# Performance work log

Hardware: AMD Instinct MI355X
Metric: run time of the kernel (lower is better)

The kernel has to match this reference:

```python
import jax, jax.numpy as jnp
import numpy as np

NS, NV = 48, 10            # scalar / vector multiplicities
IN_SIZE = NS + 3*NV + 3*NV + NS   # 156
N_EDGE_FEAT = 96
HIDDEN = 96
# weight shapes per output irrep: 0e:(58,48) 1o:(68,10) 1e:(68,10) 0o:(58,48)
W_SHAPES = [('0e', NS + NV, NS), ('1o', NS + 2*NV, NV), ('1e', 2*NV + NS, NV), ('0o', NV + NS, NS)]
WEIGHT_NUMEL = sum(a*b for _, a, b in W_SHAPES)  # 6928
N_NODES, N_EDGES = 10000, 50000


def setup_inputs() -> dict:
    key = jax.random.key(0)
    ks = jax.random.split(key, 9)
    node_attr = jax.random.normal(ks[0], (N_NODES, IN_SIZE), dtype=jnp.float32)
    edge_index = jax.random.randint(ks[1], (2, N_EDGES), 0, N_NODES)
    edge_attr = jax.random.normal(ks[2], (N_EDGES, N_EDGE_FEAT), dtype=jnp.float32)
    edge_sh = jax.random.normal(ks[3], (N_EDGES, 4), dtype=jnp.float32)
    s1 = 1.0 / np.sqrt(N_EDGE_FEAT)
    s2 = 1.0 / np.sqrt(HIDDEN)
    W1 = jax.random.normal(ks[4], (N_EDGE_FEAT, HIDDEN), dtype=jnp.float32) * s1
    b1 = jnp.zeros((HIDDEN,), dtype=jnp.float32)
    W2 = jax.random.normal(ks[5], (HIDDEN, WEIGHT_NUMEL), dtype=jnp.float32) * s2
    b2 = jnp.zeros((WEIGHT_NUMEL,), dtype=jnp.float32)
    return {'node_attr': node_attr, 'edge_index': edge_index, 'edge_attr': edge_attr,
            'edge_sh': edge_sh, 'W1': W1, 'b1': b1, 'W2': W2, 'b2': b2}


def _faster_tp(in_, sh, weight):
    # in_: [E, 156], sh: [E, 4], weight: [E, 6928]
    in_0e = in_[:, :NS]                                   # [E,48]
    in_1o = in_[:, NS:NS + 3*NV].reshape(-1, NV, 3)       # [E,10,3]
    in_1e = in_[:, NS + 3*NV:NS + 6*NV].reshape(-1, NV, 3)
    in_0o = in_[:, NS + 6*NV:]                            # [E,48]
    sh_0e = sh[:, 0]                                      # [E]
    sh_1o = sh[:, 1:]                                     # [E,3]
    inv_s3 = 1.0 / np.sqrt(3.0)
    inv_s2 = 1.0 / np.sqrt(2.0)

    out_0e = jnp.concatenate([
        in_0e * sh_0e[:, None],
        jnp.sum(in_1o * sh_1o[:, None, :], axis=-1) * inv_s3], axis=-1)      # [E,58]
    out_1o = jnp.concatenate([
        in_0e[:, :, None] * sh_1o[:, None, :],
        in_1o * sh_0e[:, None, None],
        jnp.cross(in_1e, sh_1o[:, None, :]) * inv_s2], axis=-2)              # [E,68,3]
    out_1e = jnp.concatenate([
        jnp.cross(in_1o, sh_1o[:, None, :]) * inv_s2,
        in_1e * sh_0e[:, None, None],
        in_0o[:, :, None] * sh_1o[:, None, :]], axis=-2)                     # [E,68,3]
    out_0o = jnp.concatenate([
        jnp.sum(in_1e * sh_1o[:, None, :], axis=-1) * inv_s3,
        in_0o * sh_0e[:, None]], axis=-1)                                    # [E,58]

    wd = {}
    start = 0
    for name, a, b in W_SHAPES:
        wd[name] = weight[:, start:start + a*b].reshape(-1, a, b) / np.sqrt(a)
        start += a*b

    o0e = jnp.einsum('ei,eio->eo', out_0e, wd['0e'])                 # [E,48]
    o1o = jnp.einsum('eic,eio->eoc', out_1o, wd['1o']).reshape(-1, 3*NV)
    o1e = jnp.einsum('eic,eio->eoc', out_1e, wd['1e']).reshape(-1, 3*NV)
    o0o = jnp.einsum('ei,eio->eo', out_0o, wd['0o'])                 # [E,48]
    return jnp.concatenate([o0e, o1o, o1e, o0o], axis=-1)           # [E,156]


def reference(node_attr, edge_index, edge_attr, edge_sh, W1, b1, W2, b2):
    edge_src, edge_dst = edge_index[0], edge_index[1]
    # edge MLP -> per-edge TP weights
    h = jax.nn.relu(edge_attr @ W1 + b1)
    w = h @ W2 + b2                                       # [E, 6928]
    tp = _faster_tp(node_attr[edge_dst], edge_sh, w)      # [E, 156]
    # scatter-mean over source nodes
    n = node_attr.shape[0]
    seg = jax.ops.segment_sum(tp, edge_src, num_segments=n)
    cnt = jax.ops.segment_sum(jnp.ones((tp.shape[0],), tp.dtype), edge_src, num_segments=n)
    out = seg / jnp.maximum(cnt, 1.0)[:, None]
    # residual (in/out sizes equal, so pad is a no-op)
    return out + node_attr
```

## Files before the change

kernel.cpp:

```cpp
#include <hip/hip_runtime.h>

#define NE 50000
#define NN 10000
#define KH 96
#define WN 6928
#define NTILE 484
#define IN_SZ 156
#define EPW 64

typedef __attribute__((ext_vector_type(8))) short short8;
typedef __attribute__((ext_vector_type(4))) float float4v;

__device__ __forceinline__ unsigned short f2bf(float x) {
  unsigned u = __float_as_uint(x);
  unsigned r = (u + 0x7FFFu + ((u >> 16) & 1u)) >> 16;
  return (unsigned short)r;
}
__device__ __forceinline__ float b2f(unsigned short u) {
  return __uint_as_float(((unsigned)u) << 16);
}

__device__ __forceinline__ void issue3(short8 (&B)[3], float &bv,
                                       const unsigned short* p, const float* pb) {
  asm volatile("global_load_dwordx4 %0, %4, off\n\t"
               "global_load_dwordx4 %1, %4, off offset:1024\n\t"
               "global_load_dwordx4 %2, %4, off offset:2048\n\t"
               "global_load_dword %3, %5, off"
               : "=&v"(B[0]), "=&v"(B[1]), "=&v"(B[2]), "=&v"(bv)
               : "v"(p), "v"(pb));
}
__device__ __forceinline__ void waitB8(short8 (&B)[3], float &bv) {
  asm volatile("s_waitcnt vmcnt(8)"
               : "+v"(B[0]), "+v"(B[1]), "+v"(B[2]), "+v"(bv));
}
__device__ __forceinline__ void waitB4(short8 (&B)[3], float &bv) {
  asm volatile("s_waitcnt vmcnt(4)"
               : "+v"(B[0]), "+v"(B[1]), "+v"(B[2]), "+v"(bv));
}
__device__ __forceinline__ void waitB0(short8 (&B)[3], float &bv) {
  asm volatile("s_waitcnt vmcnt(0)"
               : "+v"(B[0]), "+v"(B[1]), "+v"(B[2]), "+v"(bv));
}

__device__ __forceinline__ int col_of_np(int np) {
  if (np < 2784) return np;
  if (np < 3872) { int rel = np - 2784, i = rel >> 4, o = rel & 15; return (o < 10) ? 2784 + i * 10 + o : -1; }
  if (np < 4960) { int rel = np - 3872, i = rel >> 4, o = rel & 15; return (o < 10) ? 3464 + i * 10 + o : -1; }
  return 4144 + (np - 4960);
}

#define R0 (NTILE * 192)
#define R1 (R0 + NTILE * 16)
#define R2 (R1 + KH * KH)
#define R3 (R2 + NN * IN_SZ / 4)
#define R4 (R3 + NN / 4)
#define R5 (R4 + 576)
__global__ __launch_bounds__(256) void prep_kernel(
    const float* __restrict__ W2, const float* __restrict__ b2,
    const float* __restrict__ W1,
    unsigned short* __restrict__ W2PT, float* __restrict__ b2PT,
    unsigned short* __restrict__ W1T,
    float* __restrict__ acc, int* __restrict__ icnt,
    unsigned short* __restrict__ h_ext)
{
  int gid = blockIdx.x * 256 + threadIdx.x;
  if (gid < R0) {
    int lane = gid & 63, s = (gid >> 6) % 3, t = gid / 192;
    int l = lane & 15, q = lane >> 4;
    int c = col_of_np(t * 16 + l);
    int kbase = s * 32 + q * 8;
    unsigned short o8[8];
    #pragma unroll
    for (int j = 0; j < 8; ++j) {
      int k = kbase + j;
      float v = (c >= 0) ? W2[(size_t)k * WN + c] : 0.f;
      o8[j] = f2bf(v);
    }
    uint4 pk;
    pk.x = o8[0] | ((unsigned)o8[1] << 16);
    pk.y = o8[2] | ((unsigned)o8[3] << 16);
    pk.z = o8[4] | ((unsigned)o8[5] << 16);
    pk.w = o8[6] | ((unsigned)o8[7] << 16);
    *(uint4*)(W2PT + (size_t)gid * 8) = pk;
  } else if (gid < R1) {
    int j = gid - R0;
    int c = col_of_np(j);
    b2PT[j] = (c >= 0) ? b2[c] : 0.f;
  } else if (gid < R2) {
    int j = gid - R1;
    int c = j / KH, k = j - c * KH;
    W1T[c * KH + k] = f2bf(W1[k * KH + c]);
  } else if (gid < R3) {
    uint4 z = {0, 0, 0, 0};
    ((uint4*)acc)[gid - R2] = z;
  } else if (gid < R4) {
    uint4 z = {0, 0, 0, 0};
    ((uint4*)icnt)[gid - R3] = z;
  } else if (gid < R5) {
    uint4 z = {0, 0, 0, 0};
    ((uint4*)(h_ext + (size_t)NE * KH))[gid - R4] = z;
  }
}

__global__ __launch_bounds__(384) void mlp1_kernel(
    const float* __restrict__ edge_attr, const unsigned short* __restrict__ W1T,
    const float* __restrict__ b1, unsigned short* __restrict__ h_ext)
{
  const int tid = threadIdx.x;
  const int e0 = blockIdx.x * 16;
  const int w = tid >> 6, l = tid & 15, q = (tid >> 4) & 3;

  short8 a[3], b[3];
  #pragma unroll
  for (int s = 0; s < 3; ++s) {
    const float* pa = edge_attr + (size_t)(e0 + l) * KH + s * 32 + q * 8;
    float4 x = *(const float4*)pa, y = *(const float4*)(pa + 4);
    short8 t;
    t[0] = (short)f2bf(x.x); t[1] = (short)f2bf(x.y);
    t[2] = (short)f2bf(x.z); t[3] = (short)f2bf(x.w);
    t[4] = (short)f2bf(y.x); t[5] = (short)f2bf(y.y);
    t[6] = (short)f2bf(y.z); t[7] = (short)f2bf(y.w);
    a[s] = t;
    b[s] = *(const short8*)(W1T + (size_t)(w * 16 + l) * KH + s * 32 + q * 8);
  }
  float4v C = {0.f, 0.f, 0.f, 0.f};
  #pragma unroll
  for (int s = 0; s < 3; ++s)
    C = __builtin_amdgcn_mfma_f32_16x16x32_bf16(a[s], b[s], C, 0, 0, 0);

  float bv = b1[w * 16 + l];
  #pragma unroll
  for (int r = 0; r < 4; ++r)
    h_ext[(size_t)(e0 + q * 4 + r) * KH + w * 16 + l] = f2bf(fmaxf(C[r] + bv, 0.f));
}

__global__ __launch_bounds__(512, 2) void tp_kernel(
    const unsigned short* __restrict__ h_ext, const float* __restrict__ node_attr,
    const int* __restrict__ edge_index, const float* __restrict__ edge_sh,
    const unsigned short* __restrict__ W2PT, const float* __restrict__ b2PT,
    float* __restrict__ acc, int* __restrict__ icnt)
{
  __shared__ unsigned short sIn[EPW][160];
  __shared__ float sOut[EPW][IN_SZ];
  __shared__ unsigned short sF0[2][60][EPW];
  __shared__ unsigned short sF1[2][68][3][EPW];
  __shared__ float sShs[EPW][4];
  __shared__ int sSrc[EPW], sDst[EPW];

  const int tid = threadIdx.x;
  const int e0 = blockIdx.x * EPW;

  if (tid < EPW) {
    int ok = (e0 + tid) < NE;
    int s = ok ? edge_index[e0 + tid] : 0;
    int d = ok ? edge_index[NE + e0 + tid] : 0;
    sSrc[tid] = s; sDst[tid] = d;
    if (ok) atomicAdd(&icnt[s], 1);
  }
  if (tid >= 128 && tid < 384) {
    int t2 = tid - 128;
    int e = t2 >> 2, c = t2 & 3;
    sShs[e][c] = ((e0 + e) < NE) ? edge_sh[(size_t)(e0 + e) * 4 + c] : 0.f;
  }
  __syncthreads();

  for (int idx = tid; idx < EPW * IN_SZ; idx += 512) {
    int e = idx / IN_SZ, f = idx - e * IN_SZ;
    sIn[e][f] = f2bf(node_attr[(size_t)sDst[e] * IN_SZ + f]);
  }
  for (int idx = tid; idx < EPW * IN_SZ; idx += 512) (&sOut[0][0])[idx] = 0.f;
  __syncthreads();

  {
    const int e = tid >> 3, j = tid & 7;
    const float sh0 = sShs[e][0], sx = sShs[e][1], sy = sShs[e][2], sz = sShs[e][3];
    const float i3 = 0.57735026918962576f, i2 = 0.70710678118654752f;
    for (int i = j; i < 48; i += 8) {
      float v0 = b2f(sIn[e][i]), w0 = b2f(sIn[e][108 + i]);
      sF0[0][i][e] = f2bf(v0 * sh0);
      sF0[1][10 + i][e] = f2bf(w0 * sh0);
      sF1[0][i][0][e] = f2bf(v0 * sx); sF1[0][i][1][e] = f2bf(v0 * sy); sF1[0][i][2][e] = f2bf(v0 * sz);
      sF1[1][20 + i][0][e] = f2bf(w0 * sx); sF1[1][20 + i][1][e] = f2bf(w0 * sy); sF1[1][20 + i][2][e] = f2bf(w0 * sz);
    }
    for (int v = j; v < 10; v += 8) {
      float ax = b2f(sIn[e][48 + 3 * v]), ay = b2f(sIn[e][48 + 3 * v + 1]), az = b2f(sIn[e][48 + 3 * v + 2]);
      float bx = b2f(sIn[e][78 + 3 * v]), by = b2f(sIn[e][78 + 3 * v + 1]), bz = b2f(sIn[e][78 + 3 * v + 2]);
      sF0[0][48 + v][e] = f2bf((ax * sx + ay * sy + az * sz) * i3);
      sF0[1][v][e]      = f2bf((bx * sx + by * sy + bz * sz) * i3);
      sF1[0][48 + v][0][e] = f2bf(ax * sh0); sF1[0][48 + v][1][e] = f2bf(ay * sh0); sF1[0][48 + v][2][e] = f2bf(az * sh0);
      sF1[0][58 + v][0][e] = f2bf((by * sz - bz * sy) * i2);
      sF1[0][58 + v][1][e] = f2bf((bz * sx - bx * sz) * i2);
      sF1[0][58 + v][2][e] = f2bf((bx * sy - by * sx) * i2);
      sF1[1][v][0][e] = f2bf((ay * sz - az * sy) * i2);
      sF1[1][v][1][e] = f2bf((az * sx - ax * sz) * i2);
      sF1[1][v][2][e] = f2bf((ax * sy - ay * sx) * i2);
      sF1[1][10 + v][0][e] = f2bf(bx * sh0); sF1[1][10 + v][1][e] = f2bf(by * sh0); sF1[1][10 + v][2][e] = f2bf(bz * sh0);
    }
  }
  if (tid < 256) {
    int fam = tid >> 7, i = 58 + ((tid >> 6) & 1), e = tid & 63;
    sF0[fam][i][e] = 0;
  }
  __syncthreads();

  const int wv = tid >> 6, l = tid & 15, q = (tid >> 4) & 3;

  short8 Af[4][3];
  #pragma unroll
  for (int m = 0; m < 4; ++m) {
    const unsigned short* ar = h_ext + (size_t)(e0 + m * 16 + l) * KH + q * 8;
    #pragma unroll
    for (int s = 0; s < 3; ++s) Af[m][s] = *(const short8*)(ar + s * 32);
  }

  const unsigned short* wlane = W2PT + (size_t)(tid & 63) * 8;
  const float* blane = b2PT + l;

  auto sbody = [&](float (&a)[4][4], const short8 (&B)[3], float bv,
                   int sf, int i) {
    ushort4 f0 = *(const ushort4*)&sF0[sf][i][q * 4];
    ushort4 f1 = *(const ushort4*)&sF0[sf][i][16 + q * 4];
    ushort4 f2 = *(const ushort4*)&sF0[sf][i][32 + q * 4];
    ushort4 f3 = *(const ushort4*)&sF0[sf][i][48 + q * 4];
    float4v C0 = {bv, bv, bv, bv}, C1 = C0, C2 = C0, C3 = C0;
    #pragma unroll
    for (int s2 = 0; s2 < 3; ++s2) {
      C0 = __builtin_amdgcn_mfma_f32_16x16x32_bf16(Af[0][s2], B[s2], C0, 0, 0, 0);
      C1 = __builtin_amdgcn_mfma_f32_16x16x32_bf16(Af[1][s2], B[s2], C1, 0, 0, 0);
      C2 = __builtin_amdgcn_mfma_f32_16x16x32_bf16(Af[2][s2], B[s2], C2, 0, 0, 0);
      C3 = __builtin_amdgcn_mfma_f32_16x16x32_bf16(Af[3][s2], B[s2], C3, 0, 0, 0);
    }
    a[0][0] += C0[0] * b2f(f0.x); a[0][1] += C0[1] * b2f(f0.y);
    a[0][2] += C0[2] * b2f(f0.z); a[0][3] += C0[3] * b2f(f0.w);
    a[1][0] += C1[0] * b2f(f1.x); a[1][1] += C1[1] * b2f(f1.y);
    a[1][2] += C1[2] * b2f(f1.z); a[1][3] += C1[3] * b2f(f1.w);
    a[2][0] += C2[0] * b2f(f2.x); a[2][1] += C2[1] * b2f(f2.y);
    a[2][2] += C2[2] * b2f(f2.z); a[2][3] += C2[3] * b2f(f2.w);
    a[3][0] += C3[0] * b2f(f3.x); a[3][1] += C3[1] * b2f(f3.y);
    a[3][2] += C3[2] * b2f(f3.z); a[3][3] += C3[3] * b2f(f3.w);
  };
  auto sflush = [&](float (&a)[4][4], int col) {
    #pragma unroll
    for (int h = 0; h < 4; ++h)
      #pragma unroll
      for (int r = 0; r < 4; ++r)
        unsafeAtomicAdd(&sOut[h * 16 + q * 4 + r][col], a[h][r]);
  };

  if (wv < 4) {
    const int sf = wv >> 1;
    const int ibeg = (wv & 1) * 30;
    const int tb = sf ? 310 : 0;
    const int obase = sf ? 108 : 0;
    #pragma unroll 1
    for (int ob = 0; ob < 3; ++ob) {
      float a[4][4] = {{0.f,0.f,0.f,0.f},{0.f,0.f,0.f,0.f},{0.f,0.f,0.f,0.f},{0.f,0.f,0.f,0.f}};
      short8 Ba[3], Bb[3], Bc[3];
      float vA, vB, vC;
      auto tadr = [&](int ii) -> size_t {
        int i = ibeg + ii; if (i >= 58) i = ibeg;
        return (size_t)(tb + 3 * i + ob);
      };
      { size_t t = tadr(0); issue3(Ba, vA, wlane + t * 1536, blane + t * 16); }
      { size_t t = tadr(1); issue3(Bb, vB, wlane + t * 1536, blane + t * 16); }
      { size_t t = tadr(2); issue3(Bc, vC, wlane + t * 1536, blane + t * 16); }
      #pragma unroll 1
      for (int ii = 0; ii < 27; ii += 3) {
        waitB8(Ba, vA); sbody(a, Ba, vA, sf, ibeg + ii);
        { size_t t = tadr(ii + 3); issue3(Ba, vA, wlane + t * 1536, blane + t * 16); }
        waitB8(Bb, vB); sbody(a, Bb, vB, sf, ibeg + ii + 1);
        { size_t t = tadr(ii + 4); issue3(Bb, vB, wlane + t * 1536, blane + t * 16); }
        waitB8(Bc, vC); sbody(a, Bc, vC, sf, ibeg + ii + 2);
        { size_t t = tadr(ii + 5); issue3(Bc, vC, wlane + t * 1536, blane + t * 16); }
      }
      waitB8(Ba, vA); sbody(a, Ba, vA, sf, ibeg + 27);
      waitB4(Bb, vB); sbody(a, Bb, vB, sf, ibeg + 28);
      waitB0(Bc, vC); sbody(a, Bc, vC, sf, ibeg + 29);
      sflush(a, obase + ob * 16 + l);
    }
  } else {
    const int vf = (wv >> 1) - 2;
    const int ibeg = (wv & 1) * 34;
    const int tb = vf ? 242 : 174;
    float r0[4][3] = {{0.f}}, r1[4][3] = {{0.f}}, r2[4][3] = {{0.f}}, r3[4][3] = {{0.f}};
    short8 Ba[3], Bb[3];
    float vA, vB;
    auto tadr = [&](int ii) -> size_t { return (size_t)(tb + ibeg + ii); };
    auto vbody = [&](const short8 (&B)[3], float bv, int ii) {
      int i = ibeg + ii;
      ushort4 g0[3], g1[3], g2[3], g3[3];
      #pragma unroll
      for (int cc = 0; cc < 3; ++cc) {
        g0[cc] = *(const ushort4*)&sF1[vf][i][cc][q * 4];
        g1[cc] = *(const ushort4*)&sF1[vf][i][cc][16 + q * 4];
        g2[cc] = *(const ushort4*)&sF1[vf][i][cc][32 + q * 4];
        g3[cc] = *(const ushort4*)&sF1[vf][i][cc][48 + q * 4];
      }
      float4v C0 = {bv, bv, bv, bv}, C1 = C0, C2 = C0, C3 = C0;
      #pragma unroll
      for (int s = 0; s < 3; ++s) {
        C0 = __builtin_amdgcn_mfma_f32_16x16x32_bf16(Af[0][s], B[s], C0, 0, 0, 0);
        C1 = __builtin_amdgcn_mfma_f32_16x16x32_bf16(Af[1][s], B[s], C1, 0, 0, 0);
        C2 = __builtin_amdgcn_mfma_f32_16x16x32_bf16(Af[2][s], B[s], C2, 0, 0, 0);
        C3 = __builtin_amdgcn_mfma_f32_16x16x32_bf16(Af[3][s], B[s], C3, 0, 0, 0);
      }
      #pragma unroll
      for (int cc = 0; cc < 3; ++cc) {
        r0[0][cc] += C0[0] * b2f(g0[cc].x); r0[1][cc] += C0[1] * b2f(g0[cc].y);
        r0[2][cc] += C0[2] * b2f(g0[cc].z); r0[3][cc] += C0[3] * b2f(g0[cc].w);
        r1[0][cc] += C1[0] * b2f(g1[cc].x); r1[1][cc] += C1[1] * b2f(g1[cc].y);
        r1[2][cc] += C1[2] * b2f(g1[cc].z); r1[3][cc] += C1[3] * b2f(g1[cc].w);
        r2[0][cc] += C2[0] * b2f(g2[cc].x); r2[1][cc] += C2[1] * b2f(g2[cc].y);
        r2[2][cc] += C2[2] * b2f(g2[cc].z); r2[3][cc] += C2[3] * b2f(g2[cc].w);
        r3[0][cc] += C3[0] * b2f(g3[cc].x); r3[1][cc] += C3[1] * b2f(g3[cc].y);
        r3[2][cc] += C3[2] * b2f(g3[cc].z); r3[3][cc] += C3[3] * b2f(g3[cc].w);
      }
    };
    { size_t t = tadr(0); issue3(Ba, vA, wlane + t * 1536, blane + t * 16); }
    { size_t t = tadr(1); issue3(Bb, vB, wlane + t * 1536, blane + t * 16); }
    #pragma unroll 1
    for (int ii = 0; ii < 32; ii += 2) {
      waitB4(Ba, vA); vbody(Ba, vA, ii);
      { size_t t = tadr(ii + 2); issue3(Ba, vA, wlane + t * 1536, blane + t * 16); }
      waitB4(Bb, vB); vbody(Bb, vB, ii + 1);
      { size_t t = tadr(ii + 3); issue3(Bb, vB, wlane + t * 1536, blane + t * 16); }
    }
    waitB4(Ba, vA); vbody(Ba, vA, 32);
    waitB0(Bb, vB); vbody(Bb, vB, 33);
    if (l < 10) {
      const int col = (vf ? 78 : 48) + 3 * l;
      #pragma unroll
      for (int r = 0; r < 4; ++r)
        #pragma unroll
        for (int cc = 0; cc < 3; ++cc) {
          unsafeAtomicAdd(&sOut[q * 4 + r][col + cc],      r0[r][cc]);
          unsafeAtomicAdd(&sOut[16 + q * 4 + r][col + cc], r1[r][cc]);
          unsafeAtomicAdd(&sOut[32 + q * 4 + r][col + cc], r2[r][cc]);
          unsafeAtomicAdd(&sOut[48 + q * 4 + r][col + cc], r3[r][cc]);
        }
    }
  }
  __syncthreads();

  const float n58 = 0.13130643285972254f, n68 = 0.12126781251816650f;
  for (int idx = tid; idx < EPW * IN_SZ; idx += 512) {
    int e = idx / IN_SZ, o = idx - e * IN_SZ;
    if (e0 + e < NE) {
      float nrm = (o < 48 || o >= 108) ? n58 : n68;
      unsafeAtomicAdd(&acc[(size_t)sSrc[e] * IN_SZ + o], sOut[e][o] * nrm);
    }
  }
}

__global__ __launch_bounds__(256) void finalize_kernel(
    const float* __restrict__ acc, const int* __restrict__ icnt,
    const float* __restrict__ node_attr, float* __restrict__ out)
{
  int idx = blockIdx.x * 256 + threadIdx.x;
  if (idx < NN * IN_SZ) {
    int n = idx / IN_SZ;
    out[idx] = acc[idx] / fmaxf((float)icnt[n], 1.f) + node_attr[idx];
  }
}

extern "C" void kernel_launch(void* const* d_in, const int* in_sizes, int n_in,
                              void* d_out, int out_size, void* d_ws, size_t ws_size,
                              hipStream_t stream)
{
  const float* node_attr  = (const float*)d_in[0];
  const int*   edge_index = (const int*)d_in[1];
  const float* edge_attr  = (const float*)d_in[2];
  const float* edge_sh    = (const float*)d_in[3];
  const float* W1 = (const float*)d_in[4];
  const float* b1 = (const float*)d_in[5];
  const float* W2 = (const float*)d_in[6];
  const float* b2 = (const float*)d_in[7];
  float* out = (float*)d_out;

  unsigned short* h_ext = (unsigned short*)d_ws;
  unsigned short* W2PT  = h_ext + (size_t)50048 * KH;
  float* b2PT = (float*)(W2PT + (size_t)NTILE * 1536);
  float* acc  = b2PT + (size_t)NTILE * 16;
  int*   icnt = (int*)(acc + (size_t)NN * IN_SZ);
  unsigned short* W1T = (unsigned short*)(icnt + NN);

  prep_kernel<<<(R5 + 255) / 256, 256, 0, stream>>>(W2, b2, W1, W2PT, b2PT, W1T,
                                                    acc, icnt, h_ext);
  mlp1_kernel<<<NE / 16, 384, 0, stream>>>(edge_attr, W1T, b1, h_ext);
  tp_kernel<<<(NE + EPW - 1) / EPW, 512, 0, stream>>>(h_ext, node_attr, edge_index,
                                                      edge_sh, W2PT, b2PT, acc, icnt);
  finalize_kernel<<<(NN * IN_SZ + 255) / 256, 256, 0, stream>>>(acc, icnt, node_attr, out);
}
```

Before: 351.3 us.

## Drop shared staging buffers; read node features directly and atomically accumulate to global

Removes the sIn staging of gathered node features and the sOut shared accumulation tile. Features are now read straight from global memory during feature construction, and per-edge partial results are atomically added straight into the global accumulator with normalization applied in registers. Padding edges are routed to an extra dummy row so no bounds check is needed. This cuts shared memory use and a barrier, which may raise occupancy, but it raises global atomic traffic because each output element is now hit from several waves separately.

```diff
diff --git a/kernel.cpp b/kernel.cpp
--- a/kernel.cpp
+++ b/kernel.cpp
@@ -52,7 +52,7 @@
 #define R0 (NTILE * 192)
 #define R1 (R0 + NTILE * 16)
 #define R2 (R1 + KH * KH)
-#define R3 (R2 + NN * IN_SZ / 4)
+#define R3 (R2 + (NN + 1) * IN_SZ / 4)
 #define R4 (R3 + NN / 4)
 #define R5 (R4 + 576)
 __global__ __launch_bounds__(256) void prep_kernel(
@@ -140,8 +140,6 @@
     const unsigned short* __restrict__ W2PT, const float* __restrict__ b2PT,
     float* __restrict__ acc, int* __restrict__ icnt)
 {
-  __shared__ unsigned short sIn[EPW][160];
-  __shared__ float sOut[EPW][IN_SZ];
   __shared__ unsigned short sF0[2][60][EPW];
   __shared__ unsigned short sF1[2][68][3][EPW];
   __shared__ float sShs[EPW][4];
@@ -152,7 +150,7 @@
 
   if (tid < EPW) {
     int ok = (e0 + tid) < NE;
-    int s = ok ? edge_index[e0 + tid] : 0;
+    int s = ok ? edge_index[e0 + tid] : NN;
     int d = ok ? edge_index[NE + e0 + tid] : 0;
     sSrc[tid] = s; sDst[tid] = d;
     if (ok) atomicAdd(&icnt[s], 1);
@@ -164,27 +162,21 @@
   }
   __syncthreads();
 
-  for (int idx = tid; idx < EPW * IN_SZ; idx += 512) {
-    int e = idx / IN_SZ, f = idx - e * IN_SZ;
-    sIn[e][f] = f2bf(node_attr[(size_t)sDst[e] * IN_SZ + f]);
-  }
-  for (int idx = tid; idx < EPW * IN_SZ; idx += 512) (&sOut[0][0])[idx] = 0.f;
-  __syncthreads();
-
   {
     const int e = tid >> 3, j = tid & 7;
+    const float* na = node_attr + (size_t)sDst[e] * IN_SZ;
     const float sh0 = sShs[e][0], sx = sShs[e][1], sy = sShs[e][2], sz = sShs[e][3];
     const float i3 = 0.57735026918962576f, i2 = 0.70710678118654752f;
     for (int i = j; i < 48; i += 8) {
-      float v0 = b2f(sIn[e][i]), w0 = b2f(sIn[e][108 + i]);
+      float v0 = na[i], w0 = na[108 + i];
       sF0[0][i][e] = f2bf(v0 * sh0);
       sF0[1][10 + i][e] = f2bf(w0 * sh0);
       sF1[0][i][0][e] = f2bf(v0 * sx); sF1[0][i][1][e] = f2bf(v0 * sy); sF1[0][i][2][e] = f2bf(v0 * sz);
       sF1[1][20 + i][0][e] = f2bf(w0 * sx); sF1[1][20 + i][1][e] = f2bf(w0 * sy); sF1[1][20 + i][2][e] = f2bf(w0 * sz);
     }
     for (int v = j; v < 10; v += 8) {
-      float ax = b2f(sIn[e][48 + 3 * v]), ay = b2f(sIn[e][48 + 3 * v + 1]), az = b2f(sIn[e][48 + 3 * v + 2]);
-      float bx = b2f(sIn[e][78 + 3 * v]), by = b2f(sIn[e][78 + 3 * v + 1]), bz = b2f(sIn[e][78 + 3 * v + 2]);
+      float ax = na[48 + 3 * v], ay = na[48 + 3 * v + 1], az = na[48 + 3 * v + 2];
+      float bx = na[78 + 3 * v], by = na[78 + 3 * v + 1], bz = na[78 + 3 * v + 2];
       sF0[0][48 + v][e] = f2bf((ax * sx + ay * sy + az * sz) * i3);
       sF0[1][v][e]      = f2bf((bx * sx + by * sy + bz * sz) * i3);
       sF1[0][48 + v][0][e] = f2bf(ax * sh0); sF1[0][48 + v][1][e] = f2bf(ay * sh0); sF1[0][48 + v][2][e] = f2bf(az * sh0);
@@ -204,6 +196,7 @@
   __syncthreads();
 
   const int wv = tid >> 6, l = tid & 15, q = (tid >> 4) & 3;
+  const float n58 = 0.13130643285972254f, n68 = 0.12126781251816650f;
 
   short8 Af[4][3];
   #pragma unroll
@@ -243,8 +236,10 @@
     #pragma unroll
     for (int h = 0; h < 4; ++h)
       #pragma unroll
-      for (int r = 0; r < 4; ++r)
-        unsafeAtomicAdd(&sOut[h * 16 + q * 4 + r][col], a[h][r]);
+      for (int r = 0; r < 4; ++r) {
+        int el = h * 16 + q * 4 + r;
+        unsafeAtomicAdd(&acc[(size_t)sSrc[el] * IN_SZ + col], a[h][r] * n58);
+      }
   };
 
   if (wv < 4) {
@@ -330,24 +325,15 @@
     if (l < 10) {
       const int col = (vf ? 78 : 48) + 3 * l;
       #pragma unroll
-      for (int r = 0; r < 4; ++r)
+      for (int r = 0; r < 4; ++r) {
         #pragma unroll
         for (int cc = 0; cc < 3; ++cc) {
-          unsafeAtomicAdd(&sOut[q * 4 + r][col + cc],      r0[r][cc]);
-          unsafeAtomicAdd(&sOut[16 + q * 4 + r][col + cc], r1[r][cc]);
-          unsafeAtomicAdd(&sOut[32 + q * 4 + r][col + cc], r2[r][cc]);
-          unsafeAtomicAdd(&sOut[48 + q * 4 + r][col + cc], r3[r][cc]);
+          unsafeAtomicAdd(&acc[(size_t)sSrc[q * 4 + r] * IN_SZ + col + cc],      r0[r][cc] * n68);
+          unsafeAtomicAdd(&acc[(size_t)sSrc[16 + q * 4 + r] * IN_SZ + col + cc], r1[r][cc] * n68);
+          unsafeAtomicAdd(&acc[(size_t)sSrc[32 + q * 4 + r] * IN_SZ + col + cc], r2[r][cc] * n68);
+          unsafeAtomicAdd(&acc[(size_t)sSrc[48 + q * 4 + r] * IN_SZ + col + cc], r3[r][cc] * n68);
         }
-    }
-  }
-  __syncthreads();
-
-  const float n58 = 0.13130643285972254f, n68 = 0.12126781251816650f;
-  for (int idx = tid; idx < EPW * IN_SZ; idx += 512) {
-    int e = idx / IN_SZ, o = idx - e * IN_SZ;
-    if (e0 + e < NE) {
-      float nrm = (o < 48 || o >= 108) ? n58 : n68;
-      unsafeAtomicAdd(&acc[(size_t)sSrc[e] * IN_SZ + o], sOut[e][o] * nrm);
+      }
     }
   }
 }
@@ -381,7 +367,7 @@
   unsigned short* W2PT  = h_ext + (size_t)50048 * KH;
   float* b2PT = (float*)(W2PT + (size_t)NTILE * 1536);
   float* acc  = b2PT + (size_t)NTILE * 16;
-  int*   icnt = (int*)(acc + (size_t)NN * IN_SZ);
+  int*   icnt = (int*)(acc + (size_t)(NN + 1) * IN_SZ);
   unsigned short* W1T = (unsigned short*)(icnt + NN);
 
   prep_kernel<<<(R5 + 255) / 256, 256, 0, stream>>>(W2, b2, W1, W2PT, b2PT, W1T,
```

Result: faster. 332.6 us (-5.3%).
